# Kernel tuning notes

Measured on AMD Instinct MI355X. Metric: run time of the kernel, lower is better.

## Reference

```python
import jax, jax.numpy as jnp
import numpy as np

C = 512
GROUPS = 32
EPS = 1e-6


def setup_inputs() -> dict:
    key = jax.random.key(0)
    ks = jax.random.split(key, 10)
    s = 0.02
    return {
        "x": jax.random.normal(ks[0], (2, C, 64, 64), dtype=jnp.float32),
        "gn_scale": jnp.ones((C,), jnp.float32),
        "gn_bias": jnp.zeros((C,), jnp.float32),
        "wq": jax.random.normal(ks[1], (C, C), jnp.float32) * s,
        "bq": jnp.zeros((C,), jnp.float32),
        "wk": jax.random.normal(ks[2], (C, C), jnp.float32) * s,
        "bk": jnp.zeros((C,), jnp.float32),
        "wv": jax.random.normal(ks[3], (C, C), jnp.float32) * s,
        "bv": jnp.zeros((C,), jnp.float32),
        "wo": jax.random.normal(ks[4], (C, C), jnp.float32) * s,
        "bo": jnp.zeros((C,), jnp.float32),
    }


def group_norm(x, scale, bias):
    # x: [b, c, h, w]; 32 groups over channel dim
    b, c, h, w = x.shape
    xg = x.reshape(b, GROUPS, c // GROUPS, h, w)
    mean = jnp.mean(xg, axis=(2, 3, 4), keepdims=True)
    var = jnp.var(xg, axis=(2, 3, 4), keepdims=True)
    xg = (xg - mean) * jax.lax.rsqrt(var + EPS)
    x = xg.reshape(b, c, h, w)
    return x * scale[None, :, None, None] + bias[None, :, None, None]


def reference(x, gn_scale, gn_bias, wq, bq, wk, bk, wv, bv, wo, bo):
    b, c, h, w = x.shape
    n = h * w
    hn = group_norm(x, gn_scale, gn_bias).reshape(b, c, n)  # [b,c,n]
    # 1x1 conv == channel matmul: out[b,o,n] = W[o,i] @ h[b,i,n] + bias
    q = jnp.einsum('oi,bin->bon', wq, hn) + bq[None, :, None]
    k = jnp.einsum('oi,bin->bon', wk, hn) + bk[None, :, None]
    v = jnp.einsum('oi,bin->bon', wv, hn) + bv[None, :, None]
    # weight[b, i, j] = q_i . k_j, softmax over j
    scale = int(c) ** (-0.5)
    weight = jnp.einsum('bci,bcj->bij', q, k) * scale  # [b,n,n]
    weight = jax.nn.softmax(weight, axis=2)
    # h[b,c,i] = sum_j v[b,c,j] * weight[b,i,j]
    out = jnp.einsum('bcj,bij->bci', v, weight)
    out = jnp.einsum('oi,bin->bon', wo, out) + bo[None, :, None]
    return out.reshape(b, c, h, w) + x
```

## Files before the change

### kernel.cpp

```cpp
#include <hip/hip_runtime.h>
#include <hip/hip_bf16.h>


typedef __attribute__((ext_vector_type(8))) short short8_t;
typedef __attribute__((ext_vector_type(4))) short short4_t;
typedef __attribute__((ext_vector_type(4))) float f32x4;

__device__ __forceinline__ void gload16(const void* g, void* l) {
  __builtin_amdgcn_global_load_lds(
      (const __attribute__((address_space(1))) void*)g,
      (__attribute__((address_space(3))) void*)l, 16, 0, 0);
}

__device__ __forceinline__ short f2bf_bits(float f) {
  __hip_bfloat16 h = __float2bfloat16(f);
  return *reinterpret_cast<short*>(&h);
}
__device__ __forceinline__ float bfbits2f(short s) {
  union { unsigned int u; float f; } c;
  c.u = ((unsigned int)(unsigned short)s) << 16;
  return c.f;
}

__global__ __launch_bounds__(512)
void s_gemm8(const __hip_bfloat16* __restrict__ qk,
             __hip_bfloat16* __restrict__ P, float* __restrict__ part2,
             float c)
{
  const long long QKz = 4096LL * 1024;
  const long long SS  = 4096LL * 4096;

  const int b = blockIdx.x;
  const int bz = b >> 8;
  const int r = b & 255, xcd = r & 7, sl = r >> 3;
  const int bm = (xcd >> 1) * 4 + (sl & 3);
  const int bn = (xcd & 1) * 8 + (sl >> 2);

  const __hip_bfloat16* Aq = qk + (size_t)bz * QKz;
  const __hip_bfloat16* Bk = Aq + 512;

  const int tid = threadIdx.x;
  const int wid = tid >> 6, l = tid & 63;
  const int wrM = wid >> 2, wcN = wid & 3;
  const int lhi = l >> 4, llo = l & 15;

  __shared__ char sm[2 * 65536];

  f32x4 acc[2][2][4][2] = {};
  short8_t af[4][2], bf[2][2];

  const int rIn = l >> 3;
  const int colSw = 8 * ((l & 7) ^ (rIn & 7));
  const __hip_bfloat16* gA = Aq + (size_t)(bm * 256 + rIn) * 1024 + colSw;
  const __hip_bfloat16* gB = Bk + (size_t)(bn * 256 + rIn) * 1024 + colSw;

  auto STG = [&](int mat, int half, int t) {
    const __hip_bfloat16* src = mat ? gB : gA;
    char* dst = sm + (t & 1) * 65536 + mat * 32768;
    const int rb = half * 128 + wid * 16;
    gload16(src + (size_t)rb * 1024 + t * 64, dst + rb * 128);
    gload16(src + (size_t)(rb + 8) * 1024 + t * 64, dst + (rb + 8) * 128);
  };

#define PHASE(MH, NH, LA, LB, VM, ...) do {                                   \
    const char* bbA = sm + bsel * 65536;                                      \
    const char* bbB = bbA + 32768;                                            \
    if (LA) {                                                                 \
      _Pragma("unroll") for (int m = 0; m < 4; ++m) {                         \
        const int rowA = (MH) * 128 + wrM * 64 + m * 16 + llo;                \
        _Pragma("unroll") for (int kk = 0; kk < 2; ++kk)                      \
          af[m][kk] = *(const short8_t*)(bbA + rowA * 128 +                   \
                        (((kk * 4 + lhi) ^ (rowA & 7)) * 16));                \
      }                                                                       \
    }                                                                         \
    if (LB) {                                                                 \
      _Pragma("unroll") for (int n = 0; n < 2; ++n) {                         \
        const int rowB = (NH) * 128 + wcN * 32 + n * 16 + llo;                \
        _Pragma("unroll") for (int kk = 0; kk < 2; ++kk)                      \
          bf[n][kk] = *(const short8_t*)(bbB + rowB * 128 +                   \
                        (((kk * 4 + lhi) ^ (rowB & 7)) * 16));                \
      }                                                                       \
    }                                                                         \
    __VA_ARGS__;                                                              \
    __builtin_amdgcn_s_barrier();                                             \
    __builtin_amdgcn_s_setprio(1);                                            \
    _Pragma("unroll") for (int kk = 0; kk < 2; ++kk)                          \
      _Pragma("unroll") for (int m = 0; m < 4; ++m)                           \
        _Pragma("unroll") for (int n = 0; n < 2; ++n)                         \
          acc[MH][NH][m][n] = __builtin_amdgcn_mfma_f32_16x16x32_bf16(        \
              af[m][kk], bf[n][kk], acc[MH][NH][m][n], 0, 0, 0);              \
    __builtin_amdgcn_s_setprio(0);                                            \
    if ((VM) == 1) asm volatile("s_waitcnt vmcnt(4)" ::: "memory");           \
    if ((VM) == 2) asm volatile("s_waitcnt vmcnt(0)" ::: "memory");           \
    __builtin_amdgcn_s_barrier();                                             \
  } while (0)

  STG(0, 0, 0); STG(1, 0, 0); STG(0, 1, 0); STG(1, 1, 0);
  STG(0, 0, 1); STG(1, 0, 1); STG(0, 1, 1); STG(1, 1, 1);
  asm volatile("s_waitcnt vmcnt(0)" ::: "memory");
  __builtin_amdgcn_s_barrier();

  for (int t = 0; t < 8; ++t) {
    const int bsel = t & 1;
    const int stB = (t >= 1 && t < 7);
    const int stA = (t < 6);
    const int vm = (t < 6) ? 1 : (t == 6) ? 2 : 0;
    PHASE(0, 0, 1, 1, 0, if (stB) { STG(1, 0, t + 1); STG(1, 1, t + 1); });
    PHASE(0, 1, 0, 1, 0, if (stA) STG(0, 0, t + 2););
    PHASE(1, 1, 1, 0, 0, );
    PHASE(1, 0, 0, 1, vm, if (stA) STG(0, 1, t + 2););
  }
#undef PHASE

  __hip_bfloat16* Pb = P + (size_t)bz * SS;
  float rp[2][4][4];
#pragma unroll
  for (int Mh = 0; Mh < 2; ++Mh)
#pragma unroll
    for (int m = 0; m < 4; ++m)
#pragma unroll
      for (int rr = 0; rr < 4; ++rr) {
        const int grow = bm * 256 + Mh * 128 + wrM * 64 + m * 16 + lhi * 4 + rr;
        float s = 0.f;
#pragma unroll
        for (int Nh = 0; Nh < 2; ++Nh)
#pragma unroll
          for (int n = 0; n < 2; ++n) {
            const int gcol = bn * 256 + Nh * 128 + wcN * 32 + n * 16 + llo;
            const float v = exp2f(acc[Mh][Nh][m][n][rr] * c);
            Pb[(size_t)grow * 4096 + gcol] = __float2bfloat16(v);
            s += v;
          }
        rp[Mh][m][rr] = s;
      }
#pragma unroll
  for (int Mh = 0; Mh < 2; ++Mh)
#pragma unroll
    for (int m = 0; m < 4; ++m)
#pragma unroll
      for (int rr = 0; rr < 4; ++rr) {
        float s = rp[Mh][m][rr];
        s += __shfl_xor(s, 1); s += __shfl_xor(s, 2);
        s += __shfl_xor(s, 4); s += __shfl_xor(s, 8);
        rp[Mh][m][rr] = s;
      }
  __syncthreads();
  float* rsl = (float*)sm;
  if (llo == 0) {
#pragma unroll
    for (int Mh = 0; Mh < 2; ++Mh)
#pragma unroll
      for (int m = 0; m < 4; ++m)
#pragma unroll
        for (int rr = 0; rr < 4; ++rr) {
          const int rl = Mh * 128 + wrM * 64 + m * 16 + lhi * 4 + rr;
          rsl[rl * 4 + wcN] = rp[Mh][m][rr];
        }
  }
  __syncthreads();
  if (tid < 256) {
    const float s = rsl[tid * 4] + rsl[tid * 4 + 1] + rsl[tid * 4 + 2] + rsl[tid * 4 + 3];
    part2[((size_t)bz * 16 + bn) * 4096 + bm * 256 + tid] = s;
  }
}

__global__ __launch_bounds__(256)
void rs_final(const float* __restrict__ part2, float* __restrict__ rs)
{
  const int i = blockIdx.x * 256 + threadIdx.x;
  const int z = i >> 12, row = i & 4095;
  float s = 0.f;
#pragma unroll
  for (int bn = 0; bn < 16; ++bn)
    s += part2[((size_t)z * 16 + bn) * 4096 + row];
  rs[(size_t)z * 4096 + row] = 1.f / s;
}

template<int OUTF, int BIASMODE, int RESID, int PIPE, int SWZ, int MF, int NORM>
__global__ __launch_bounds__(256, 2)
void gemm_nt(const __hip_bfloat16* __restrict__ A,
             const __hip_bfloat16* __restrict__ B,
             void* __restrict__ Cv,
             const float* __restrict__ bias,
             const float* __restrict__ resid,
             const float* __restrict__ rnorm,
             float scale, int M, int N, int K,
             int lda, int ldb, int ldc,
             long long strA, long long strB, long long strC, long long strR)
{
  int bm, bn, bz;
  if (SWZ == 0) {
    bm = blockIdx.x; bn = blockIdx.y; bz = blockIdx.z;
  } else if (SWZ == 2) {
    const int b = blockIdx.x;
    bz = b >> 10;
    const int b2 = b & 1023;
    const int xcd = b2 & 7, s = b2 >> 3;
    bm = (xcd >> 1) * 8 + (s & 7);
    bn = (xcd & 1) * 16 + (s >> 3);
  } else {
    const int b = blockIdx.x;
    const int xcd = b & 7, slot = b >> 3;
    bm = slot & 7;
    const int panel = xcd * 8 + (slot >> 3);
    bn = panel & 31; bz = panel >> 5;
  }
  const int z = bz;
  A += (size_t)z * strA;
  B += (size_t)z * strB;

  const int tid = threadIdx.x;
  const int w = tid >> 6, l = tid & 63;
  const int wr = w >> 1, wc = w & 1;
  const int lhi = l >> 4, llo = l & 15;
  const int m0 = bm * (MF * 32), n0 = bn * 128;

  constexpr int BUFSZ = MF * 4096 + 16384;
  __shared__ char sm[(PIPE ? 2 : 1) * BUFSZ];

  f32x4 acc[MF][4] = {};

  const int rowInCh = l >> 3;
  const int colOff = 8 * ((l & 7) ^ (rowInCh & 7));

  const __hip_bfloat16* gAr[MF];
  const __hip_bfloat16* gBr[4];
#pragma unroll
  for (int j = 0; j < MF; ++j)
    gAr[j] = A + (size_t)(m0 + w * (8 * MF) + j * 8 + rowInCh) * lda + colOff;
#pragma unroll
  for (int r = 0; r < 4; ++r)
    gBr[r] = B + (size_t)(n0 + w * 32 + r * 8 + rowInCh) * ldb + colOff;

  auto stage = [&](int kt, int buf) {
    char* sA = sm + buf * BUFSZ;
    char* sB = sA + MF * 4096;
    const int ko = kt * 64;
#pragma unroll
    for (int j = 0; j < MF; ++j)
      gload16(gAr[j] + ko, sA + (w * MF + j) * 1024);
#pragma unroll
    for (int r = 0; r < 4; ++r)
      gload16(gBr[r] + ko, sB + (w * 4 + r) * 1024);
  };

  auto compute = [&](int buf) {
    char* sA = sm + buf * BUFSZ;
    char* sB = sA + MF * 4096;
#pragma unroll
    for (int kk = 0; kk < 2; ++kk) {
      short8_t af[MF], bfv[4];
#pragma unroll
      for (int m = 0; m < MF; ++m) {
        const int row = wr * (16 * MF) + m * 16 + llo;
        const int inner = ((kk * 4 + lhi) ^ (row & 7)) * 16;
        af[m] = *(const short8_t*)(sA + row * 128 + inner);
      }
#pragma unroll
      for (int n = 0; n < 4; ++n) {
        const int row = wc * 64 + n * 16 + llo;
        const int inner = ((kk * 4 + lhi) ^ (row & 7)) * 16;
        bfv[n] = *(const short8_t*)(sB + row * 128 + inner);
      }
#pragma unroll
      for (int m = 0; m < MF; ++m)
#pragma unroll
        for (int n = 0; n < 4; ++n)
          acc[m][n] = __builtin_amdgcn_mfma_f32_16x16x32_bf16(af[m], bfv[n], acc[m][n], 0, 0, 0);
    }
  };

  const int nkt = K >> 6;
  if (PIPE) {
    stage(0, 0);
    __syncthreads();
    int cur = 0;
    for (int kt = 0; kt < nkt; ++kt) {
      if (kt + 1 < nkt) stage(kt + 1, cur ^ 1);
      compute(cur);
      __syncthreads();
      cur ^= 1;
    }
  } else {
    for (int kt = 0; kt < nkt; ++kt) {
      __syncthreads();
      stage(kt, 0);
      __syncthreads();
      compute(0);
    }
  }

#pragma unroll
  for (int m = 0; m < MF; ++m) {
#pragma unroll
    for (int r = 0; r < 4; ++r) {
      const int grow = m0 + wr * (16 * MF) + m * 16 + lhi * 4 + r;
#pragma unroll
      for (int n = 0; n < 4; ++n) {
        const int gcol = n0 + wc * 64 + n * 16 + llo;
        float v = acc[m][n][r] * scale;
        if (NORM) v *= rnorm[(size_t)z * 4096 + gcol];
        if (BIASMODE == 1) v += bias[grow];
        if (BIASMODE == 2) v += bias[gcol];
        const size_t idx = (size_t)z * strC + (size_t)grow * ldc + gcol;
        if (RESID) v += resid[(size_t)z * strR + (size_t)grow * ldc + gcol];
        if (OUTF == 0) ((__hip_bfloat16*)Cv)[idx] = __float2bfloat16(v);
        else           ((float*)Cv)[idx] = v;
      }
    }
  }
}

__global__ __launch_bounds__(256)
void gn_partial(const float* __restrict__ x, float* __restrict__ part)
{
  const int g = blockIdx.x, sl = blockIdx.y, z = blockIdx.z;
  const int tid = threadIdx.x;
  const float* xf = x + (size_t)z * 512 * 4096 + (size_t)g * 16 * 4096 + (size_t)sl * 4096;
  const float4* px = reinterpret_cast<const float4*>(xf);
  float s = 0.f, q = 0.f;
#pragma unroll
  for (int i = 0; i < 4; ++i) {
    float4 v = px[tid + i * 256];
    s += v.x + v.y + v.z + v.w;
    q += v.x * v.x + v.y * v.y + v.z * v.z + v.w * v.w;
  }
#pragma unroll
  for (int o = 32; o; o >>= 1) { s += __shfl_xor(s, o); q += __shfl_xor(q, o); }
  __shared__ float rs[4], rq[4];
  if ((tid & 63) == 0) { rs[tid >> 6] = s; rq[tid >> 6] = q; }
  __syncthreads();
  if (tid == 0) {
    s = rs[0] + rs[1] + rs[2] + rs[3];
    q = rq[0] + rq[1] + rq[2] + rq[3];
    part[(((size_t)z * 32 + g) * 16 + sl) * 2 + 0] = s;
    part[(((size_t)z * 32 + g) * 16 + sl) * 2 + 1] = q;
  }
}

__global__ __launch_bounds__(64)
void gn_finalize(const float* __restrict__ part, float* __restrict__ stats, int n)
{
  const int i = threadIdx.x;
  if (i >= n) return;
  float s = 0.f, q = 0.f;
#pragma unroll
  for (int sl = 0; sl < 16; ++sl) {
    s += part[(i * 16 + sl) * 2 + 0];
    q += part[(i * 16 + sl) * 2 + 1];
  }
  const float mean = s * (1.0f / 65536.0f);
  const float var = q * (1.0f / 65536.0f) - mean * mean;
  stats[i * 2 + 0] = mean;
  stats[i * 2 + 1] = rsqrtf(var + 1e-6f);
}

__global__ __launch_bounds__(256)
void gn_apply_t(const float* __restrict__ x, const float* __restrict__ stats,
                const float* __restrict__ gns, const float* __restrict__ gnb,
                __hip_bfloat16* __restrict__ ht)
{
  const int st = blockIdx.x, ct = blockIdx.y, z = blockIdx.z;
  const int tid = threadIdx.x;
  __shared__ float tile[64][65];
  const float* xb = x + (size_t)z * 512 * 4096;
  const int lane64 = tid & 63, rr = tid >> 6;
#pragma unroll
  for (int pp = 0; pp < 16; ++pp) {
    const int cl = pp * 4 + rr;
    const int c = ct * 64 + cl;
    const int g = c >> 4;
    const float mean = stats[(z * 32 + g) * 2 + 0];
    const float rstd = stats[(z * 32 + g) * 2 + 1];
    const float val = xb[(size_t)c * 4096 + st * 64 + lane64];
    tile[cl][lane64] = (val - mean) * rstd * gns[c] + gnb[c];
  }
  __syncthreads();
  __hip_bfloat16* hb = ht + (size_t)z * 4096 * 512;
#pragma unroll
  for (int pp = 0; pp < 16; ++pp) {
    const int sl = pp * 4 + rr;
    const int s = st * 64 + sl;
    hb[(size_t)s * 512 + ct * 64 + lane64] = __float2bfloat16(tile[lane64][sl]);
  }
}

__global__ __launch_bounds__(256)
void softmax_rows(__hip_bfloat16* __restrict__ S, long long strZ)
{
  const int row = blockIdx.x, z = blockIdx.y;
  __hip_bfloat16* p = S + (size_t)z * strZ + (size_t)row * 4096;
  const int tid = threadIdx.x;
  short8_t a = *(const short8_t*)(p + tid * 16);
  short8_t b = *(const short8_t*)(p + tid * 16 + 8);
  float v[16];
#pragma unroll
  for (int i = 0; i < 8; ++i) { v[i] = bfbits2f(a[i]); v[8 + i] = bfbits2f(b[i]); }
  float m = v[0];
#pragma unroll
  for (int i = 1; i < 16; ++i) m = fmaxf(m, v[i]);
#pragma unroll
  for (int o = 32; o; o >>= 1) m = fmaxf(m, __shfl_xor(m, o));
  __shared__ float red[8];
  if ((tid & 63) == 0) red[tid >> 6] = m;
  __syncthreads();
  m = fmaxf(fmaxf(red[0], red[1]), fmaxf(red[2], red[3]));
  float s = 0.f;
#pragma unroll
  for (int i = 0; i < 16; ++i) { v[i] = exp2f((v[i] - m) * 1.44269504f); s += v[i]; }
#pragma unroll
  for (int o = 32; o; o >>= 1) s += __shfl_xor(s, o);
  __syncthreads();
  if ((tid & 63) == 0) red[4 + (tid >> 6)] = s;
  __syncthreads();
  s = red[4] + red[5] + red[6] + red[7];
  const float inv = 1.f / s;
#pragma unroll
  for (int i = 0; i < 8; ++i) { a[i] = f2bf_bits(v[i] * inv); b[i] = f2bf_bits(v[8 + i] * inv); }
  *(short8_t*)(p + tid * 16) = a;
  *(short8_t*)(p + tid * 16 + 8) = b;
}

__global__ __launch_bounds__(256)
void cast3(const float* __restrict__ w0, const float* __restrict__ w1,
           const float* __restrict__ w2, __hip_bfloat16* __restrict__ out)
{
  const int j = blockIdx.y;
  const float* src = (j == 0) ? w0 : (j == 1) ? w1 : w2;
  const int i = blockIdx.x * 256 + threadIdx.x;
  float4 v = reinterpret_cast<const float4*>(src)[i];
  short4_t o;
  o[0] = f2bf_bits(v.x); o[1] = f2bf_bits(v.y);
  o[2] = f2bf_bits(v.z); o[3] = f2bf_bits(v.w);
  *reinterpret_cast<short4_t*>((short*)out + (size_t)j * 262144 + (size_t)i * 4) = o;
}

__global__ __launch_bounds__(256)
void transpose_cast(const float* __restrict__ w, __hip_bfloat16* __restrict__ wt)
{
  __shared__ float tile[64][65];
  const int ct = blockIdx.x, it = blockIdx.y;
  const int tid = threadIdx.x;
  const int lane = tid & 63, rr = tid >> 6;
#pragma unroll
  for (int p = 0; p < 16; ++p) {
    const int cl = p * 4 + rr;
    tile[cl][lane] = w[(size_t)(ct * 64 + cl) * 512 + it * 64 + lane];
  }
  __syncthreads();
#pragma unroll
  for (int p = 0; p < 16; ++p) {
    const int il = p * 4 + rr;
    wt[(size_t)(it * 64 + il) * 512 + ct * 64 + lane] = __float2bfloat16(tile[lane][il]);
  }
}

__global__ __launch_bounds__(64)
void prep_bias(const float* __restrict__ wo, const float* __restrict__ bv,
               const float* __restrict__ bo, const float* __restrict__ bq,
               const float* __restrict__ bk,
               float* __restrict__ bvo, float* __restrict__ bqk)
{
  const int o = blockIdx.x * 64 + threadIdx.x;
  const float4* row = reinterpret_cast<const float4*>(wo + (size_t)o * 512);
  const float4* b4 = reinterpret_cast<const float4*>(bv);
  float s = 0.f;
#pragma unroll 8
  for (int i = 0; i < 128; ++i) {
    float4 a = row[i], b = b4[i];
    s += a.x * b.x + a.y * b.y + a.z * b.z + a.w * b.w;
  }
  bvo[o] = s + bo[o];
  bqk[o] = bq[o];
  bqk[512 + o] = bk[o];
}

extern "C" void kernel_launch(void* const* d_in, const int* in_sizes, int n_in,
                              void* d_out, int out_size, void* d_ws, size_t ws_size,
                              hipStream_t stream)
{
  const float* x   = (const float*)d_in[0];
  const float* gns = (const float*)d_in[1];
  const float* gnb = (const float*)d_in[2];
  const float* wq  = (const float*)d_in[3];
  const float* bq  = (const float*)d_in[4];
  const float* wk  = (const float*)d_in[5];
  const float* bk  = (const float*)d_in[6];
  const float* wv  = (const float*)d_in[7];
  const float* bv  = (const float*)d_in[8];
  const float* wo  = (const float*)d_in[9];
  const float* bo  = (const float*)d_in[10];
  float* out = (float*)d_out;

  const int WB = 512 * 512;
  const long long HT  = 4096LL * 512;
  const long long QKz = 4096LL * 1024;
  const long long VOz = 512LL * 4096;
  const long long SS  = 4096LL * 4096;
  const long long CHW = 512LL * 4096;

  char* base = (char*)d_ws;
  size_t off = 0;
  auto alloc = [&](size_t b) { void* r = base + off; off = (off + b + 255) & ~(size_t)255; return r; };

  __hip_bfloat16* wbf = (__hip_bfloat16*)alloc((size_t)5 * WB * 2);
  float* bqk   = (float*)alloc(1024 * 4);
  float* bvo   = (float*)alloc(512 * 4);
  float* part  = (float*)alloc(2 * 32 * 16 * 2 * 4);
  float* stats = (float*)alloc(2 * 32 * 2 * 4);
  float* rsum  = (float*)alloc(2 * 4096 * 4);
  float* part2 = (float*)alloc((size_t)2 * 16 * 4096 * 4);
  const size_t fixed = off;

  const size_t qkB = (size_t)2 * QKz * 2;
  const size_t voB = (size_t)2 * VOz * 2;
  const size_t sB2 = (size_t)2 * SS * 2;
  const size_t sB1 = (size_t)SS * 2;
  const int MODE = (ws_size >= fixed + qkB + voB + sB2) ? 2 : 1;

  __hip_bfloat16* qk   = (__hip_bfloat16*)alloc(qkB);
  __hip_bfloat16* vo   = (__hip_bfloat16*)alloc(voB);
  const size_t sbufB = (MODE == 2) ? sB2 : sB1;
  __hip_bfloat16* sbuf = (__hip_bfloat16*)alloc(sbufB);
  __hip_bfloat16* ht = (__hip_bfloat16*)((char*)sbuf + sbufB - (size_t)2 * HT * 2);

  __hip_bfloat16* wqk = wbf;
  __hip_bfloat16* woB = wbf + 2 * WB;
  __hip_bfloat16* wvT = wbf + 3 * WB;
  __hip_bfloat16* wvo = wbf + 4 * WB;

  const float SC = 0.04419417382415922f;
  const float CEXP = SC * 1.4426950408889634f;

  cast3<<<dim3(256, 3), 256, 0, stream>>>(wq, wk, wo, wbf);
  transpose_cast<<<dim3(8, 8), 256, 0, stream>>>(wv, wvT);
  prep_bias<<<8, 64, 0, stream>>>(wo, bv, bo, bq, bk, bvo, bqk);
  gn_partial<<<dim3(32, 16, 2), 256, 0, stream>>>(x, part);
  gn_finalize<<<1, 64, 0, stream>>>(part, stats, 64);

  gemm_nt<0, 0, 0, 1, 0, 4, 0><<<dim3(4, 4, 1), 256, 0, stream>>>(
      woB, wvT, wvo, nullptr, nullptr, nullptr, 1.f, 512, 512, 512,
      512, 512, 512, 0, 0, 0, 0);

  gn_apply_t<<<dim3(64, 8, 2), 256, 0, stream>>>(x, stats, gns, gnb, ht);

  gemm_nt<0, 2, 0, 1, 0, 4, 0><<<dim3(32, 8, 2), 256, 0, stream>>>(
      ht, wqk, qk, bqk, nullptr, nullptr, 1.f, 4096, 1024, 512,
      512, 512, 1024, HT, 0, QKz, 0);

  gemm_nt<0, 0, 0, 1, 3, 2, 0><<<dim3(512, 1, 1), 256, 0, stream>>>(
      wvo, ht, vo, nullptr, nullptr, nullptr, 1.f, 512, 4096, 512,
      512, 512, 4096, 0, HT, VOz, 0);

  if (MODE == 2) {
    s_gemm8<<<512, 512, 0, stream>>>(qk, sbuf, part2, CEXP);
    rs_final<<<32, 256, 0, stream>>>(part2, rsum);
    gemm_nt<1, 1, 1, 1, 3, 2, 1><<<dim3(512, 1, 1), 256, 0, stream>>>(
        vo, sbuf, out, bvo, x, rsum, 1.f, 512, 4096, 4096,
        4096, 4096, 4096, VOz, SS, CHW, CHW);
  } else {
    for (int z = 0; z < 2; ++z) {
      gemm_nt<0, 0, 0, 0, 0, 4, 0><<<dim3(32, 32, 1), 256, 0, stream>>>(
          qk + (size_t)z * QKz, qk + (size_t)z * QKz + 512, sbuf, nullptr, nullptr,
          nullptr, SC, 4096, 4096, 512, 1024, 1024, 4096, 0, 0, 0, 0);
      softmax_rows<<<dim3(4096, 1), 256, 0, stream>>>(sbuf, 0);
      gemm_nt<1, 1, 1, 1, 0, 2, 0><<<dim3(8, 32, 1), 256, 0, stream>>>(
          vo + (size_t)z * VOz, sbuf, out + (size_t)z * CHW, bvo, x + (size_t)z * CHW,
          nullptr, 1.f, 512, 4096, 4096, 4096, 4096, 4096, 0, 0, 0, 0);
    }
  }
}
```

Baseline: 156.3 us.

## Merge small prep kernels, fuse QK and VO GEMMs, inline row-sum finalize

Combines the weight cast, the wv transpose, the bias prep and the groupnorm partial sums into one prep_all launch. The groupnorm finalize moves into gn_apply_t, and the reciprocal row-sum reduction moves into the prologue of the output GEMM, which removes the gn_finalize and rs_final launches. The QK and VO projection GEMMs are merged into a single 1024-block launch so they run concurrently. The aim is fewer kernel launches and less serialization between tail blocks, at the cost of redundant per-block reductions and a 64KB static shared allocation in the fused GEMM kernel, which may limit occupancy.

Result: no change. 153.7 us (-1.7%).

```diff
diff --git a/kernel.cpp b/kernel.cpp
--- a/kernel.cpp
+++ b/kernel.cpp
@@ -164,16 +164,127 @@
   }
 }
 
-__global__ __launch_bounds__(256)
-void rs_final(const float* __restrict__ part2, float* __restrict__ rs)
-{
-  const int i = blockIdx.x * 256 + threadIdx.x;
-  const int z = i >> 12, row = i & 4095;
-  float s = 0.f;
-#pragma unroll
-  for (int bn = 0; bn < 16; ++bn)
-    s += part2[((size_t)z * 16 + bn) * 4096 + row];
-  rs[(size_t)z * 4096 + row] = 1.f / s;
+template<int OUTF, int BIASMODE, int RESID, int PIPE, int MF, int NORM>
+__device__ __forceinline__ void gemm_body(
+    const __hip_bfloat16* __restrict__ A,
+    const __hip_bfloat16* __restrict__ B,
+    void* __restrict__ Cv,
+    const float* __restrict__ bias,
+    const float* __restrict__ resid,
+    const float* __restrict__ p2,
+    float scale, int K, int lda, int ldb, int ldc,
+    long long strC, long long strR,
+    int bm, int bn, int z, char* sm, float* rsn)
+{
+  constexpr int BUFSZ = MF * 4096 + 16384;
+  const int tid = threadIdx.x;
+  const int w = tid >> 6, l = tid & 63;
+  const int wr = w >> 1, wc = w & 1;
+  const int lhi = l >> 4, llo = l & 15;
+  const int m0 = bm * (MF * 32), n0 = bn * 128;
+
+  if (NORM == 2) {
+    if (tid < 128) {
+      float s = 0.f;
+#pragma unroll
+      for (int bb = 0; bb < 16; ++bb)
+        s += p2[((size_t)z * 16 + bb) * 4096 + n0 + tid];
+      rsn[tid] = 1.f / s;
+    }
+    __syncthreads();
+  }
+
+  f32x4 acc[MF][4] = {};
+
+  const int rowInCh = l >> 3;
+  const int colOff = 8 * ((l & 7) ^ (rowInCh & 7));
+
+  const __hip_bfloat16* gAr[MF];
+  const __hip_bfloat16* gBr[4];
+#pragma unroll
+  for (int j = 0; j < MF; ++j)
+    gAr[j] = A + (size_t)(m0 + w * (8 * MF) + j * 8 + rowInCh) * lda + colOff;
+#pragma unroll
+  for (int r = 0; r < 4; ++r)
+    gBr[r] = B + (size_t)(n0 + w * 32 + r * 8 + rowInCh) * ldb + colOff;
+
+  auto stage = [&](int kt, int buf) {
+    char* sA = sm + buf * BUFSZ;
+    char* sB = sA + MF * 4096;
+    const int ko = kt * 64;
+#pragma unroll
+    for (int j = 0; j < MF; ++j)
+      gload16(gAr[j] + ko, sA + (w * MF + j) * 1024);
+#pragma unroll
+    for (int r = 0; r < 4; ++r)
+      gload16(gBr[r] + ko, sB + (w * 4 + r) * 1024);
+  };
+
+  auto compute = [&](int buf) {
+    char* sA = sm + buf * BUFSZ;
+    char* sB = sA + MF * 4096;
+#pragma unroll
+    for (int kk = 0; kk < 2; ++kk) {
+      short8_t af[MF], bfv[4];
+#pragma unroll
+      for (int m = 0; m < MF; ++m) {
+        const int row = wr * (16 * MF) + m * 16 + llo;
+        const int inner = ((kk * 4 + lhi) ^ (row & 7)) * 16;
+        af[m] = *(const short8_t*)(sA + row * 128 + inner);
+      }
+#pragma unroll
+      for (int n = 0; n < 4; ++n) {
+        const int row = wc * 64 + n * 16 + llo;
+        const int inner = ((kk * 4 + lhi) ^ (row & 7)) * 16;
+        bfv[n] = *(const short8_t*)(sB + row * 128 + inner);
+      }
+#pragma unroll
+      for (int m = 0; m < MF; ++m)
+#pragma unroll
+        for (int n = 0; n < 4; ++n)
+          acc[m][n] = __builtin_amdgcn_mfma_f32_16x16x32_bf16(af[m], bfv[n], acc[m][n], 0, 0, 0);
+    }
+  };
+
+  const int nkt = K >> 6;
+  if (PIPE) {
+    stage(0, 0);
+    __syncthreads();
+    int cur = 0;
+    for (int kt = 0; kt < nkt; ++kt) {
+      if (kt + 1 < nkt) stage(kt + 1, cur ^ 1);
+      compute(cur);
+      __syncthreads();
+      cur ^= 1;
+    }
+  } else {
+    for (int kt = 0; kt < nkt; ++kt) {
+      __syncthreads();
+      stage(kt, 0);
+      __syncthreads();
+      compute(0);
+    }
+  }
+
+#pragma unroll
+  for (int m = 0; m < MF; ++m) {
+#pragma unroll
+    for (int r = 0; r < 4; ++r) {
+      const int grow = m0 + wr * (16 * MF) + m * 16 + lhi * 4 + r;
+#pragma unroll
+      for (int n = 0; n < 4; ++n) {
+        const int gcol = n0 + wc * 64 + n * 16 + llo;
+        float v = acc[m][n][r] * scale;
+        if (NORM == 2) v *= rsn[wc * 64 + n * 16 + llo];
+        if (BIASMODE == 1) v += bias[grow];
+        if (BIASMODE == 2) v += bias[gcol];
+        const size_t idx = (size_t)z * strC + (size_t)grow * ldc + gcol;
+        if (RESID) v += resid[(size_t)z * strR + (size_t)grow * ldc + gcol];
+        if (OUTF == 0) ((__hip_bfloat16*)Cv)[idx] = __float2bfloat16(v);
+        else           ((float*)Cv)[idx] = v;
+      }
+    }
+  }
 }
 
 template<int OUTF, int BIASMODE, int RESID, int PIPE, int SWZ, int MF, int NORM>
@@ -183,7 +294,7 @@
              void* __restrict__ Cv,
              const float* __restrict__ bias,
              const float* __restrict__ resid,
-             const float* __restrict__ rnorm,
+             const float* __restrict__ p2,
              float scale, int M, int N, int K,
              int lda, int ldb, int ldc,
              long long strA, long long strB, long long strC, long long strR)
@@ -205,175 +316,148 @@
     const int panel = xcd * 8 + (slot >> 3);
     bn = panel & 31; bz = panel >> 5;
   }
-  const int z = bz;
-  A += (size_t)z * strA;
-  B += (size_t)z * strB;
-
-  const int tid = threadIdx.x;
-  const int w = tid >> 6, l = tid & 63;
-  const int wr = w >> 1, wc = w & 1;
-  const int lhi = l >> 4, llo = l & 15;
-  const int m0 = bm * (MF * 32), n0 = bn * 128;
-
-  constexpr int BUFSZ = MF * 4096 + 16384;
-  __shared__ char sm[(PIPE ? 2 : 1) * BUFSZ];
-
-  f32x4 acc[MF][4] = {};
-
-  const int rowInCh = l >> 3;
-  const int colOff = 8 * ((l & 7) ^ (rowInCh & 7));
-
-  const __hip_bfloat16* gAr[MF];
-  const __hip_bfloat16* gBr[4];
-#pragma unroll
-  for (int j = 0; j < MF; ++j)
-    gAr[j] = A + (size_t)(m0 + w * (8 * MF) + j * 8 + rowInCh) * lda + colOff;
-#pragma unroll
-  for (int r = 0; r < 4; ++r)
-    gBr[r] = B + (size_t)(n0 + w * 32 + r * 8 + rowInCh) * ldb + colOff;
-
-  auto stage = [&](int kt, int buf) {
-    char* sA = sm + buf * BUFSZ;
-    char* sB = sA + MF * 4096;
-    const int ko = kt * 64;
-#pragma unroll
-    for (int j = 0; j < MF; ++j)
-      gload16(gAr[j] + ko, sA + (w * MF + j) * 1024);
-#pragma unroll
-    for (int r = 0; r < 4; ++r)
-      gload16(gBr[r] + ko, sB + (w * 4 + r) * 1024);
-  };
-
-  auto compute = [&](int buf) {
-    char* sA = sm + buf * BUFSZ;
-    char* sB = sA + MF * 4096;
-#pragma unroll
-    for (int kk = 0; kk < 2; ++kk) {
-      short8_t af[MF], bfv[4];
-#pragma unroll
-      for (int m = 0; m < MF; ++m) {
-        const int row = wr * (16 * MF) + m * 16 + llo;
-        const int inner = ((kk * 4 + lhi) ^ (row & 7)) * 16;
-        af[m] = *(const short8_t*)(sA + row * 128 + inner);
-      }
-#pragma unroll
-      for (int n = 0; n < 4; ++n) {
-        const int row = wc * 64 + n * 16 + llo;
-        const int inner = ((kk * 4 + lhi) ^ (row & 7)) * 16;
-        bfv[n] = *(const short8_t*)(sB + row * 128 + inner);
-      }
-#pragma unroll
-      for (int m = 0; m < MF; ++m)
-#pragma unroll
-        for (int n = 0; n < 4; ++n)
-          acc[m][n] = __builtin_amdgcn_mfma_f32_16x16x32_bf16(af[m], bfv[n], acc[m][n], 0, 0, 0);
-    }
-  };
-
-  const int nkt = K >> 6;
-  if (PIPE) {
-    stage(0, 0);
+  __shared__ char sm[(PIPE ? 2 : 1) * (MF * 4096 + 16384)];
+  __shared__ float rsn[128];
+  gemm_body<OUTF, BIASMODE, RESID, PIPE, MF, NORM>(
+      A + (size_t)bz * strA, B + (size_t)bz * strB, Cv, bias, resid, p2,
+      scale, K, lda, ldb, ldc, strC, strR, bm, bn, bz, sm, rsn);
+}
+
+__global__ __launch_bounds__(256, 2)
+void qkvo(const __hip_bfloat16* __restrict__ ht,
+          const __hip_bfloat16* __restrict__ wqk,
+          const __hip_bfloat16* __restrict__ wvo,
+          __hip_bfloat16* __restrict__ qk,
+          __hip_bfloat16* __restrict__ vo,
+          const float* __restrict__ bqk)
+{
+  const long long HT  = 4096LL * 512;
+  const long long QKz = 4096LL * 1024;
+  const long long VOz = 512LL * 4096;
+  __shared__ char sm[65536];
+  const int b = blockIdx.x;
+  if (b < 512) {
+    const int bm = b & 31, bn = (b >> 5) & 7, bz = b >> 8;
+    gemm_body<0, 2, 0, 1, 4, 0>(
+        ht + (size_t)bz * HT, wqk, qk, bqk, nullptr, nullptr,
+        1.f, 512, 512, 512, 1024, QKz, 0, bm, bn, bz, sm, nullptr);
+  } else {
+    const int b2 = b - 512;
+    const int xcd = b2 & 7, slot = b2 >> 3;
+    const int bm = slot & 7;
+    const int panel = xcd * 8 + (slot >> 3);
+    const int bn = panel & 31, bz = panel >> 5;
+    gemm_body<0, 0, 0, 1, 2, 0>(
+        wvo, ht + (size_t)bz * HT, vo, nullptr, nullptr, nullptr,
+        1.f, 512, 512, 512, 4096, VOz, 0, bm, bn, bz, sm, nullptr);
+  }
+}
+
+__global__ __launch_bounds__(256)
+void prep_all(const float* __restrict__ wq, const float* __restrict__ wk,
+              const float* __restrict__ wo, const float* __restrict__ wv,
+              const float* __restrict__ bv, const float* __restrict__ bo,
+              const float* __restrict__ bq, const float* __restrict__ bk,
+              const float* __restrict__ x,
+              __hip_bfloat16* __restrict__ wbf, __hip_bfloat16* __restrict__ wvT,
+              float* __restrict__ bvo, float* __restrict__ bqk,
+              float* __restrict__ part)
+{
+  const int b = blockIdx.x, tid = threadIdx.x;
+  if (b < 768) {
+    const int j = b >> 8;
+    const float* src = (j == 0) ? wq : (j == 1) ? wk : wo;
+    const int i = (b & 255) * 256 + tid;
+    float4 v = reinterpret_cast<const float4*>(src)[i];
+    short4_t o;
+    o[0] = f2bf_bits(v.x); o[1] = f2bf_bits(v.y);
+    o[2] = f2bf_bits(v.z); o[3] = f2bf_bits(v.w);
+    *reinterpret_cast<short4_t*>((short*)wbf + (size_t)j * 262144 + (size_t)i * 4) = o;
+  } else if (b < 832) {
+    __shared__ float tile[64][65];
+    const int b2 = b - 768, ct = b2 >> 3, it = b2 & 7;
+    const int lane = tid & 63, rr = tid >> 6;
+#pragma unroll
+    for (int p = 0; p < 16; ++p) {
+      const int cl = p * 4 + rr;
+      tile[cl][lane] = wv[(size_t)(ct * 64 + cl) * 512 + it * 64 + lane];
+    }
     __syncthreads();
-    int cur = 0;
-    for (int kt = 0; kt < nkt; ++kt) {
-      if (kt + 1 < nkt) stage(kt + 1, cur ^ 1);
-      compute(cur);
-      __syncthreads();
-      cur ^= 1;
-    }
+#pragma unroll
+    for (int p = 0; p < 16; ++p) {
+      const int il = p * 4 + rr;
+      wvT[(size_t)(it * 64 + il) * 512 + ct * 64 + lane] = __float2bfloat16(tile[lane][il]);
+    }
+  } else if (b < 834) {
+    const int o = (b - 832) * 256 + tid;
+    const float4* row = reinterpret_cast<const float4*>(wo + (size_t)o * 512);
+    const float4* b4 = reinterpret_cast<const float4*>(bv);
+    float s = 0.f;
+#pragma unroll 8
+    for (int i = 0; i < 128; ++i) {
+      float4 a = row[i], bb = b4[i];
+      s += a.x * bb.x + a.y * bb.y + a.z * bb.z + a.w * bb.w;
+    }
+    bvo[o] = s + bo[o];
+    bqk[o] = bq[o];
+    bqk[512 + o] = bk[o];
   } else {
-    for (int kt = 0; kt < nkt; ++kt) {
-      __syncthreads();
-      stage(kt, 0);
-      __syncthreads();
-      compute(0);
-    }
-  }
-
-#pragma unroll
-  for (int m = 0; m < MF; ++m) {
-#pragma unroll
-    for (int r = 0; r < 4; ++r) {
-      const int grow = m0 + wr * (16 * MF) + m * 16 + lhi * 4 + r;
-#pragma unroll
-      for (int n = 0; n < 4; ++n) {
-        const int gcol = n0 + wc * 64 + n * 16 + llo;
-        float v = acc[m][n][r] * scale;
-        if (NORM) v *= rnorm[(size_t)z * 4096 + gcol];
-        if (BIASMODE == 1) v += bias[grow];
-        if (BIASMODE == 2) v += bias[gcol];
-        const size_t idx = (size_t)z * strC + (size_t)grow * ldc + gcol;
-        if (RESID) v += resid[(size_t)z * strR + (size_t)grow * ldc + gcol];
-        if (OUTF == 0) ((__hip_bfloat16*)Cv)[idx] = __float2bfloat16(v);
-        else           ((float*)Cv)[idx] = v;
-      }
+    const int b3 = b - 834;
+    const int g = b3 & 31, sl = (b3 >> 5) & 15, z = b3 >> 9;
+    const float* xf = x + (size_t)z * 512 * 4096 + (size_t)g * 16 * 4096 + (size_t)sl * 4096;
+    const float4* px = reinterpret_cast<const float4*>(xf);
+    float s = 0.f, q = 0.f;
+#pragma unroll
+    for (int i = 0; i < 4; ++i) {
+      float4 v = px[tid + i * 256];
+      s += v.x + v.y + v.z + v.w;
+      q += v.x * v.x + v.y * v.y + v.z * v.z + v.w * v.w;
+    }
+#pragma unroll
+    for (int o = 32; o; o >>= 1) { s += __shfl_xor(s, o); q += __shfl_xor(q, o); }
+    __shared__ float rs[4], rq[4];
+    if ((tid & 63) == 0) { rs[tid >> 6] = s; rq[tid >> 6] = q; }
+    __syncthreads();
+    if (tid == 0) {
+      s = rs[0] + rs[1] + rs[2] + rs[3];
+      q = rq[0] + rq[1] + rq[2] + rq[3];
+      part[(((size_t)z * 32 + g) * 16 + sl) * 2 + 0] = s;
+      part[(((size_t)z * 32 + g) * 16 + sl) * 2 + 1] = q;
     }
   }
 }
 
 __global__ __launch_bounds__(256)
-void gn_partial(const float* __restrict__ x, float* __restrict__ part)
-{
-  const int g = blockIdx.x, sl = blockIdx.y, z = blockIdx.z;
-  const int tid = threadIdx.x;
-  const float* xf = x + (size_t)z * 512 * 4096 + (size_t)g * 16 * 4096 + (size_t)sl * 4096;
-  const float4* px = reinterpret_cast<const float4*>(xf);
-  float s = 0.f, q = 0.f;
-#pragma unroll
-  for (int i = 0; i < 4; ++i) {
-    float4 v = px[tid + i * 256];
-    s += v.x + v.y + v.z + v.w;
-    q += v.x * v.x + v.y * v.y + v.z * v.z + v.w * v.w;
-  }
-#pragma unroll
-  for (int o = 32; o; o >>= 1) { s += __shfl_xor(s, o); q += __shfl_xor(q, o); }
-  __shared__ float rs[4], rq[4];
-  if ((tid & 63) == 0) { rs[tid >> 6] = s; rq[tid >> 6] = q; }
-  __syncthreads();
-  if (tid == 0) {
-    s = rs[0] + rs[1] + rs[2] + rs[3];
-    q = rq[0] + rq[1] + rq[2] + rq[3];
-    part[(((size_t)z * 32 + g) * 16 + sl) * 2 + 0] = s;
-    part[(((size_t)z * 32 + g) * 16 + sl) * 2 + 1] = q;
-  }
-}
-
-__global__ __launch_bounds__(64)
-void gn_finalize(const float* __restrict__ part, float* __restrict__ stats, int n)
-{
-  const int i = threadIdx.x;
-  if (i >= n) return;
-  float s = 0.f, q = 0.f;
-#pragma unroll
-  for (int sl = 0; sl < 16; ++sl) {
-    s += part[(i * 16 + sl) * 2 + 0];
-    q += part[(i * 16 + sl) * 2 + 1];
-  }
-  const float mean = s * (1.0f / 65536.0f);
-  const float var = q * (1.0f / 65536.0f) - mean * mean;
-  stats[i * 2 + 0] = mean;
-  stats[i * 2 + 1] = rsqrtf(var + 1e-6f);
-}
-
-__global__ __launch_bounds__(256)
-void gn_apply_t(const float* __restrict__ x, const float* __restrict__ stats,
+void gn_apply_t(const float* __restrict__ x, const float* __restrict__ part,
                 const float* __restrict__ gns, const float* __restrict__ gnb,
                 __hip_bfloat16* __restrict__ ht)
 {
   const int st = blockIdx.x, ct = blockIdx.y, z = blockIdx.z;
   const int tid = threadIdx.x;
   __shared__ float tile[64][65];
+  __shared__ float smean[4], srstd[4];
+  if (tid < 4) {
+    const int g = ct * 4 + tid;
+    float s = 0.f, q = 0.f;
+#pragma unroll
+    for (int slc = 0; slc < 16; ++slc) {
+      s += part[(((size_t)z * 32 + g) * 16 + slc) * 2 + 0];
+      q += part[(((size_t)z * 32 + g) * 16 + slc) * 2 + 1];
+    }
+    const float mean = s * (1.0f / 65536.0f);
+    const float var = q * (1.0f / 65536.0f) - mean * mean;
+    smean[tid] = mean;
+    srstd[tid] = rsqrtf(var + 1e-6f);
+  }
+  __syncthreads();
   const float* xb = x + (size_t)z * 512 * 4096;
   const int lane64 = tid & 63, rr = tid >> 6;
 #pragma unroll
   for (int pp = 0; pp < 16; ++pp) {
     const int cl = pp * 4 + rr;
     const int c = ct * 64 + cl;
-    const int g = c >> 4;
-    const float mean = stats[(z * 32 + g) * 2 + 0];
-    const float rstd = stats[(z * 32 + g) * 2 + 1];
     const float val = xb[(size_t)c * 4096 + st * 64 + lane64];
-    tile[cl][lane64] = (val - mean) * rstd * gns[c] + gnb[c];
+    tile[cl][lane64] = (val - smean[cl >> 4]) * srstd[cl >> 4] * gns[c] + gnb[c];
   }
   __syncthreads();
   __hip_bfloat16* hb = ht + (size_t)z * 4096 * 512;
@@ -419,60 +503,6 @@
   for (int i = 0; i < 8; ++i) { a[i] = f2bf_bits(v[i] * inv); b[i] = f2bf_bits(v[8 + i] * inv); }
   *(short8_t*)(p + tid * 16) = a;
   *(short8_t*)(p + tid * 16 + 8) = b;
-}
-
-__global__ __launch_bounds__(256)
-void cast3(const float* __restrict__ w0, const float* __restrict__ w1,
-           const float* __restrict__ w2, __hip_bfloat16* __restrict__ out)
-{
-  const int j = blockIdx.y;
-  const float* src = (j == 0) ? w0 : (j == 1) ? w1 : w2;
-  const int i = blockIdx.x * 256 + threadIdx.x;
-  float4 v = reinterpret_cast<const float4*>(src)[i];
-  short4_t o;
-  o[0] = f2bf_bits(v.x); o[1] = f2bf_bits(v.y);
-  o[2] = f2bf_bits(v.z); o[3] = f2bf_bits(v.w);
-  *reinterpret_cast<short4_t*>((short*)out + (size_t)j * 262144 + (size_t)i * 4) = o;
-}
-
-__global__ __launch_bounds__(256)
-void transpose_cast(const float* __restrict__ w, __hip_bfloat16* __restrict__ wt)
-{
-  __shared__ float tile[64][65];
-  const int ct = blockIdx.x, it = blockIdx.y;
-  const int tid = threadIdx.x;
-  const int lane = tid & 63, rr = tid >> 6;
-#pragma unroll
-  for (int p = 0; p < 16; ++p) {
-    const int cl = p * 4 + rr;
-    tile[cl][lane] = w[(size_t)(ct * 64 + cl) * 512 + it * 64 + lane];
-  }
-  __syncthreads();
-#pragma unroll
-  for (int p = 0; p < 16; ++p) {
-    const int il = p * 4 + rr;
-    wt[(size_t)(it * 64 + il) * 512 + ct * 64 + lane] = __float2bfloat16(tile[lane][il]);
-  }
-}
-
-__global__ __launch_bounds__(64)
-void prep_bias(const float* __restrict__ wo, const float* __restrict__ bv,
-               const float* __restrict__ bo, const float* __restrict__ bq,
-               const float* __restrict__ bk,
-               float* __restrict__ bvo, float* __restrict__ bqk)
-{
-  const int o = blockIdx.x * 64 + threadIdx.x;
-  const float4* row = reinterpret_cast<const float4*>(wo + (size_t)o * 512);
-  const float4* b4 = reinterpret_cast<const float4*>(bv);
-  float s = 0.f;
-#pragma unroll 8
-  for (int i = 0; i < 128; ++i) {
-    float4 a = row[i], b = b4[i];
-    s += a.x * b.x + a.y * b.y + a.z * b.z + a.w * b.w;
-  }
-  bvo[o] = s + bo[o];
-  bqk[o] = bq[o];
-  bqk[512 + o] = bk[o];
 }
 
 extern "C" void kernel_launch(void* const* d_in, const int* in_sizes, int n_in,
@@ -507,8 +537,6 @@
   float* bqk   = (float*)alloc(1024 * 4);
   float* bvo   = (float*)alloc(512 * 4);
   float* part  = (float*)alloc(2 * 32 * 16 * 2 * 4);
-  float* stats = (float*)alloc(2 * 32 * 2 * 4);
-  float* rsum  = (float*)alloc(2 * 4096 * 4);
   float* part2 = (float*)alloc((size_t)2 * 16 * 4096 * 4);
   const size_t fixed = off;
 
@@ -532,33 +560,28 @@
   const float SC = 0.04419417382415922f;
   const float CEXP = SC * 1.4426950408889634f;
 
-  cast3<<<dim3(256, 3), 256, 0, stream>>>(wq, wk, wo, wbf);
-  transpose_cast<<<dim3(8, 8), 256, 0, stream>>>(wv, wvT);
-  prep_bias<<<8, 64, 0, stream>>>(wo, bv, bo, bq, bk, bvo, bqk);
-  gn_partial<<<dim3(32, 16, 2), 256, 0, stream>>>(x, part);
-  gn_finalize<<<1, 64, 0, stream>>>(part, stats, 64);
+  prep_all<<<1858, 256, 0, stream>>>(wq, wk, wo, wv, bv, bo, bq, bk, x,
+                                     wbf, wvT, bvo, bqk, part);
 
   gemm_nt<0, 0, 0, 1, 0, 4, 0><<<dim3(4, 4, 1), 256, 0, stream>>>(
       woB, wvT, wvo, nullptr, nullptr, nullptr, 1.f, 512, 512, 512,
       512, 512, 512, 0, 0, 0, 0);
 
-  gn_apply_t<<<dim3(64, 8, 2), 256, 0, stream>>>(x, stats, gns, gnb, ht);
-
-  gemm_nt<0, 2, 0, 1, 0, 4, 0><<<dim3(32, 8, 2), 256, 0, stream>>>(
-      ht, wqk, qk, bqk, nullptr, nullptr, 1.f, 4096, 1024, 512,
-      512, 512, 1024, HT, 0, QKz, 0);
-
-  gemm_nt<0, 0, 0, 1, 3, 2, 0><<<dim3(512, 1, 1), 256, 0, stream>>>(
-      wvo, ht, vo, nullptr, nullptr, nullptr, 1.f, 512, 4096, 512,
-      512, 512, 4096, 0, HT, VOz, 0);
+  gn_apply_t<<<dim3(64, 8, 2), 256, 0, stream>>>(x, part, gns, gnb, ht);
 
   if (MODE == 2) {
+    qkvo<<<1024, 256, 0, stream>>>(ht, wqk, wvo, qk, vo, bqk);
     s_gemm8<<<512, 512, 0, stream>>>(qk, sbuf, part2, CEXP);
-    rs_final<<<32, 256, 0, stream>>>(part2, rsum);
-    gemm_nt<1, 1, 1, 1, 3, 2, 1><<<dim3(512, 1, 1), 256, 0, stream>>>(
-        vo, sbuf, out, bvo, x, rsum, 1.f, 512, 4096, 4096,
+    gemm_nt<1, 1, 1, 1, 3, 2, 2><<<dim3(512, 1, 1), 256, 0, stream>>>(
+        vo, sbuf, out, bvo, x, part2, 1.f, 512, 4096, 4096,
         4096, 4096, 4096, VOz, SS, CHW, CHW);
   } else {
+    gemm_nt<0, 2, 0, 1, 0, 4, 0><<<dim3(32, 8, 2), 256, 0, stream>>>(
+        ht, wqk, qk, bqk, nullptr, nullptr, 1.f, 4096, 1024, 512,
+        512, 512, 1024, HT, 0, QKz, 0);
+    gemm_nt<0, 0, 0, 1, 3, 2, 0><<<dim3(512, 1, 1), 256, 0, stream>>>(
+        wvo, ht, vo, nullptr, nullptr, nullptr, 1.f, 512, 4096, 512,
+        512, 512, 4096, 0, HT, VOz, 0);
     for (int z = 0; z < 2; ++z) {
       gemm_nt<0, 0, 0, 0, 0, 4, 0><<<dim3(32, 32, 1), 256, 0, stream>>>(
           qk + (size_t)z * QKz, qk + (size_t)z * QKz + 512, sbuf, nullptr, nullptr,
```
